# Performance work log

Measured on AMD Instinct MI355X. Metric: run time of the kernel, lower is better.

Reference implementation:

```python
import jax, jax.numpy as jnp
import numpy as np

B, N, E, M, H, OUT, F = 4, 10000, 160000, 4, 64, 64, 64


def setup_inputs() -> dict:
    key = jax.random.key(0)
    k1, k2, k3, k4, k5, k6 = jax.random.split(key, 6)
    node_fts = jax.random.normal(k1, (B, N, M, H), dtype=jnp.float32)
    hidden = jax.random.normal(k2, (B, N, M, H), dtype=jnp.float32)
    edge_fts = jax.random.normal(k3, (B, E, F), dtype=jnp.float32)
    edge_indices = jax.random.randint(k4, (B, E, 2), 0, N, dtype=jnp.int64)
    # hk.Linear params (truncated-normal-ish init approximated by scaled normal)
    W_nh = jax.random.normal(k5, (2 * H, OUT), dtype=jnp.float32) / np.sqrt(2 * H)
    b_nh = jnp.zeros((OUT,), dtype=jnp.float32)
    W_e = jax.random.normal(k6, (F, 1), dtype=jnp.float32) / np.sqrt(F)
    b_e = jnp.zeros((1,), dtype=jnp.float32)
    return {"node_fts": node_fts, "hidden": hidden, "edge_fts": edge_fts,
            "W_nh": W_nh, "b_nh": b_nh, "W_e": W_e, "b_e": b_e,
            "edge_indices": edge_indices}


def reference(node_fts, hidden, edge_fts, W_nh, b_nh, W_e, b_e, edge_indices):
    nb_nodes = node_fts.shape[1]
    src = edge_indices[..., 0]  # [B, E]
    tgt = edge_indices[..., 1]  # [B, E]
    # fuse node and hidden features, project: [B, N, M, 2H] @ [2H, OUT]
    nh = jnp.concatenate([node_fts, hidden], axis=-1)
    nh_fts = jnp.einsum('bnmc,co->bnmo', nh, W_nh) + b_nh  # [B, N, M, OUT]
    # gather per-edge source-node features along node axis
    nh_values = jnp.take_along_axis(nh_fts, src[:, :, None, None], axis=1)  # [B, E, M, OUT]
    # scalar gate per edge
    edge_coeff = jnp.einsum('bef,fo->beo', edge_fts, W_e) + b_e  # [B, E, 1]
    filtered = edge_coeff[..., None] * nh_values  # [B, E, M, OUT]
    # scatter-sum messages to target nodes, per batch element
    seg = jax.vmap(lambda d, s: jax.ops.segment_sum(d, s, num_segments=nb_nodes))
    updated_bits = seg(filtered, tgt)  # [B, N, M, OUT]
    return updated_bits
```

## Files before the change

kernel.cpp:

```cpp
#include <hip/hip_runtime.h>

#define Bc 4
#define Nc 10000
#define Ec 160000
#define NSEG (Bc * Nc)
#define NEDGE (Bc * Ec)
#define CAP 64
#define PROJ_BLOCKS 1250
#define GATE_BLOCKS 1250

typedef __attribute__((ext_vector_type(8))) short bf16x8;
typedef __attribute__((ext_vector_type(4))) float f32x4;

__device__ __forceinline__ unsigned short f2bf(float f) {
    union { float f; unsigned u; } x; x.f = f;
    return (unsigned short)((x.u + 0x7FFFu + ((x.u >> 16) & 1u)) >> 16);
}
__device__ __forceinline__ float bfhi(unsigned u) {
    union { unsigned u; float f; } x; x.u = u & 0xFFFF0000u; return x.f;
}
__device__ __forceinline__ float bflo(unsigned u) {
    union { unsigned u; float f; } x; x.u = u << 16; return x.f;
}

__device__ __forceinline__ float reduce16(float* p, int lane) {
#pragma unroll
    for (int off = 1, n = 8; off < 16; off <<= 1, n >>= 1) {
        const bool hi2 = (lane & off) != 0;
#pragma unroll
        for (int i = 0; i < 8; ++i)
            if (i < n) {
                const float keep = hi2 ? p[2 * i + 1] : p[2 * i];
                const float send = hi2 ? p[2 * i] : p[2 * i + 1];
                p[i] = keep + __shfl_xor(send, off, 64);
            }
    }
    return p[0];
}

__global__ __launch_bounds__(256) void proj_gate_kernel(
    const float* __restrict__ node, const float* __restrict__ hid,
    const float* __restrict__ Wnh, const float* __restrict__ bnh,
    unsigned short* __restrict__ nhf,
    const float* __restrict__ efts, const int* __restrict__ eidx,
    const float* __restrict__ We, const float* __restrict__ be,
    int2* __restrict__ epair, int slot_stride, int* __restrict__ cnt)
{
    __shared__ __align__(16) unsigned short wlds[8192];
    const int t = threadIdx.x;
    const int lane = t & 63;

    if (blockIdx.x < PROJ_BLOCKS) {
#pragma unroll
        for (int i = 0; i < 4; ++i) {
            const int f    = t + 256 * i;
            const int kt   = f >> 8;
            const int ct   = (f >> 6) & 3;
            const int l    = f & 63;
            const int quad = l >> 4, m = l & 15;
            const int col  = 16 * ct + m;
            const int krow = quad * 8 + 32 * kt;
            bf16x8 fr;
#pragma unroll
            for (int j = 0; j < 8; ++j)
                fr[j] = (short)f2bf(Wnh[(size_t)(krow + j) * 64 + col]);
            *(bf16x8*)(wlds + (size_t)f * 8) = fr;
        }
        __syncthreads();

        const int wv   = (int)(blockIdx.x * 4 + (t >> 6));
        const int m    = lane & 15;
        const int quad = lane >> 4;

        float bias[4];
#pragma unroll
        for (int ct = 0; ct < 4; ++ct) bias[ct] = bnh[m + 16 * ct];

        float4 lo[2][4], hi[2][4];
#pragma unroll
        for (int half = 0; half < 2; ++half) {
            const int arow = (wv * 2 + half) * 16 + m;
#pragma unroll
            for (int kt = 0; kt < 4; ++kt) {
                const int kbase = quad * 8 + 32 * kt;
                const float* pp = (kbase < 64)
                    ? (node + (size_t)arow * 64 + kbase)
                    : (hid  + (size_t)arow * 64 + (kbase - 64));
                lo[half][kt] = *(const float4*)pp;
                hi[half][kt] = *(const float4*)(pp + 4);
            }
        }

#pragma unroll
        for (int half = 0; half < 2; ++half) {
            f32x4 acc[4];
#pragma unroll
            for (int ct = 0; ct < 4; ++ct) acc[ct] = (f32x4){0.f, 0.f, 0.f, 0.f};
#pragma unroll
            for (int kt = 0; kt < 4; ++kt) {
                bf16x8 a;
                a[0] = (short)f2bf(lo[half][kt].x); a[1] = (short)f2bf(lo[half][kt].y);
                a[2] = (short)f2bf(lo[half][kt].z); a[3] = (short)f2bf(lo[half][kt].w);
                a[4] = (short)f2bf(hi[half][kt].x); a[5] = (short)f2bf(hi[half][kt].y);
                a[6] = (short)f2bf(hi[half][kt].z); a[7] = (short)f2bf(hi[half][kt].w);
#pragma unroll
                for (int ct = 0; ct < 4; ++ct) {
                    const bf16x8 bf = *(const bf16x8*)(wlds + (size_t)((kt * 4 + ct) * 64 + lane) * 8);
                    acc[ct] = __builtin_amdgcn_mfma_f32_16x16x32_bf16(a, bf, acc[ct], 0, 0, 0);
                }
            }
            const int r0 = (wv * 2 + half) * 16 + quad * 4;
#pragma unroll
            for (int ct = 0; ct < 4; ++ct) {
                const int col = m + 16 * ct;
#pragma unroll
                for (int reg = 0; reg < 4; ++reg)
                    nhf[(size_t)(r0 + reg) * 64 + col] = f2bf(acc[ct][reg] + bias[ct]);
            }
        }
    } else {
        const int w  = (int)((blockIdx.x - PROJ_BLOCKS) * 4 + (t >> 6));
        const int e0 = w * 128;
        const int b  = e0 / Ec;
        const int cb = b * Nc;
        const float4 w4 = *(const float4*)(We + (size_t)(lane & 15) * 4);
        const float be0 = be[0];
        const int perm = 4 * (lane & 15) + (lane >> 4);

        const int2 st0 = *(const int2*)(eidx + (size_t)(e0 + perm) * 2);
        const int2 st1 = *(const int2*)(eidx + (size_t)(e0 + 64 + perm) * 2);
        const int seg0 = cb + st0.y;
        const int seg1 = cb + st1.y;
        const int slot0 = atomicAdd(&cnt[seg0], 1);
        const int slot1 = atomicAdd(&cnt[seg1], 1);

        float4 v[16];
        const float* base0 = efts + (size_t)e0 * 64;
#pragma unroll
        for (int j = 0; j < 16; ++j)
            v[j] = *(const float4*)(base0 + (size_t)j * 256 + lane * 4);
        float p[16];
#pragma unroll
        for (int j = 0; j < 16; ++j)
            p[j] = v[j].x * w4.x + v[j].y * w4.y + v[j].z * w4.z + v[j].w * w4.w;

        const float* base1 = efts + (size_t)(e0 + 64) * 64;
#pragma unroll
        for (int j = 0; j < 16; ++j)
            v[j] = *(const float4*)(base1 + (size_t)j * 256 + lane * 4);

        {
            const float cval = reduce16(p, lane) + be0;
            if (slot0 < CAP)
                epair[(size_t)seg0 * slot_stride + slot0] = make_int2(st0.x, __float_as_int(cval));
        }

#pragma unroll
        for (int j = 0; j < 16; ++j)
            p[j] = v[j].x * w4.x + v[j].y * w4.y + v[j].z * w4.z + v[j].w * w4.w;

        {
            const float cval = reduce16(p, lane) + be0;
            if (slot1 < CAP)
                epair[(size_t)seg1 * slot_stride + slot1] = make_int2(st1.x, __float_as_int(cval));
        }
    }
}

__global__ __launch_bounds__(256) void gather_kernel(
    const int* __restrict__ cnt, const int2* epair, int slot_stride,
    const unsigned* __restrict__ nhf, float* out)
{
    const int lane = threadIdx.x & 63;
    int seg = (int)((blockIdx.x * blockDim.x + threadIdx.x) >> 6);
    if (seg >= NSEG) return;
    seg = __builtin_amdgcn_readfirstlane(seg);
    const int b = seg / Nc;
    const int deg = cnt[seg];
    const int end = deg < CAP ? deg : CAP;
    const int2* bp = epair + (size_t)seg * slot_stride;
    const unsigned* base = nhf + (size_t)b * Nc * 128 + lane * 2;
    const int2 my = bp[lane];

    f32x4 acc[4];
#pragma unroll
    for (int j = 0; j < 4; ++j) acc[j] = (f32x4){0.f, 0.f, 0.f, 0.f};

    int i = 0;
    for (; i + 8 <= end; i += 8) {
        int sx[8]; float cc[8]; uint2 r[8];
#pragma unroll
        for (int j = 0; j < 8; ++j) {
            sx[j] = __shfl(my.x, i + j, 64);
            cc[j] = __int_as_float(__shfl(my.y, i + j, 64));
        }
#pragma unroll
        for (int j = 0; j < 8; ++j) r[j] = *(const uint2*)(base + (size_t)sx[j] * 128);
#pragma unroll
        for (int j = 0; j < 8; ++j) {
            acc[j & 3][0] += cc[j] * bflo(r[j].x);
            acc[j & 3][1] += cc[j] * bfhi(r[j].x);
            acc[j & 3][2] += cc[j] * bflo(r[j].y);
            acc[j & 3][3] += cc[j] * bfhi(r[j].y);
        }
    }
    if (i + 4 <= end) {
        int sx[4]; float cc[4]; uint2 r[4];
#pragma unroll
        for (int j = 0; j < 4; ++j) {
            sx[j] = __shfl(my.x, i + j, 64);
            cc[j] = __int_as_float(__shfl(my.y, i + j, 64));
        }
#pragma unroll
        for (int j = 0; j < 4; ++j) r[j] = *(const uint2*)(base + (size_t)sx[j] * 128);
#pragma unroll
        for (int j = 0; j < 4; ++j) {
            acc[j][0] += cc[j] * bflo(r[j].x);
            acc[j][1] += cc[j] * bfhi(r[j].x);
            acc[j][2] += cc[j] * bflo(r[j].y);
            acc[j][3] += cc[j] * bfhi(r[j].y);
        }
        i += 4;
    }
    for (; i < end; ++i) {
        const int sx = __shfl(my.x, i, 64);
        const float cc = __int_as_float(__shfl(my.y, i, 64));
        const uint2 r = *(const uint2*)(base + (size_t)sx * 128);
        acc[0][0] += cc * bflo(r.x);
        acc[0][1] += cc * bfhi(r.x);
        acc[0][2] += cc * bflo(r.y);
        acc[0][3] += cc * bfhi(r.y);
    }
    float4 o;
    o.x = (acc[0][0] + acc[1][0]) + (acc[2][0] + acc[3][0]);
    o.y = (acc[0][1] + acc[1][1]) + (acc[2][1] + acc[3][1]);
    o.z = (acc[0][2] + acc[1][2]) + (acc[2][2] + acc[3][2]);
    o.w = (acc[0][3] + acc[1][3]) + (acc[2][3] + acc[3][3]);
    *(float4*)(out + (size_t)seg * 256 + lane * 4) = o;
}

__global__ __launch_bounds__(256) void edge_atomic_kernel(
    const float* __restrict__ efts, const int* __restrict__ eidx,
    const float* __restrict__ We, const float* __restrict__ be,
    const unsigned* __restrict__ nhf, float* __restrict__ out)
{
    const int lane = threadIdx.x & 63;
    const int eg   = (int)((blockIdx.x * blockDim.x + threadIdx.x) >> 6);
    if (eg >= NEDGE) return;
    const int b = eg / Ec;
    float c = efts[(size_t)eg * 64 + lane] * We[lane];
#pragma unroll
    for (int off = 32; off > 0; off >>= 1) c += __shfl_xor(c, off, 64);
    c += be[0];
    const int src = eidx[(size_t)eg * 2 + 0];
    const int tgt = eidx[(size_t)eg * 2 + 1];
    const uint2 r = *(const uint2*)(nhf + ((size_t)(b * Nc + src)) * 128 + lane * 2);
    float* op = out + ((size_t)(b * Nc + tgt)) * 256 + lane * 4;
    atomicAdd(op + 0, c * bflo(r.x));
    atomicAdd(op + 1, c * bfhi(r.x));
    atomicAdd(op + 2, c * bflo(r.y));
    atomicAdd(op + 3, c * bfhi(r.y));
}

extern "C" void kernel_launch(void* const* d_in, const int* in_sizes, int n_in,
                              void* d_out, int out_size, void* d_ws, size_t ws_size,
                              hipStream_t stream) {
    const float* node = (const float*)d_in[0];
    const float* hid  = (const float*)d_in[1];
    const float* efts = (const float*)d_in[2];
    const float* Wnh  = (const float*)d_in[3];
    const float* bnh  = (const float*)d_in[4];
    const float* We   = (const float*)d_in[5];
    const float* be   = (const float*)d_in[6];
    const int*   eidx = (const int*)d_in[7];
    float* out = (float*)d_out;

    unsigned* ws = (unsigned*)d_ws;
    unsigned short* nhf16 = (unsigned short*)ws;
    int* cnt = (int*)(ws + 5120000);
    const size_t ws_compact = (size_t)10280000 * 4;
    const size_t ws_minimal = (size_t)5160000 * 4;

    if (ws_size >= ws_minimal) {
        int2* epair;
        int stride;
        if (ws_size >= ws_compact) { epair = (int2*)(ws + 5160000); stride = 64; }
        else                       { epair = (int2*)d_out;          stride = 128; }
        hipMemsetAsync(cnt, 0, (size_t)NSEG * sizeof(int), stream);
        proj_gate_kernel<<<PROJ_BLOCKS + GATE_BLOCKS, 256, 0, stream>>>(
            node, hid, Wnh, bnh, nhf16, efts, eidx, We, be, epair, stride, cnt);
        gather_kernel<<<NSEG / 4, 256, 0, stream>>>(cnt, epair, stride, (const unsigned*)ws, out);
    } else {
        proj_gate_kernel<<<PROJ_BLOCKS, 256, 0, stream>>>(
            node, hid, Wnh, bnh, nhf16, efts, eidx, We, be,
            (int2*)d_out , 128, (int*)d_out );
        hipMemsetAsync(d_out, 0, (size_t)out_size * sizeof(float), stream);
        edge_atomic_kernel<<<NEDGE / 4, 256, 0, stream>>>(efts, eidx, We, be, (const unsigned*)ws, out);
    }
}
```

Measured before the change: 348.6 us.

## Rebalance per-wave work: finer proj/gate waves, gate-first order, two segments per gather wave

The projection branch now computes one 16-row tile per wave instead of two, and the gate branch handles 64 edges per wave instead of 128. Block counts double to compensate, and gate blocks are placed before projection blocks in the grid. The gather kernel now handles two target segments per wave in sequence, halving its grid. The goal is more parallelism and earlier scheduling of the atomic-heavy gate work, but it gives up the explicit load/compute overlap of the two-batch code. The fallback path now also launches the gate blocks, which do wasted work there.

Result: no change. 352.2 us (+1.0%).

```diff
diff --git a/kernel.cpp b/kernel.cpp
--- a/kernel.cpp
+++ b/kernel.cpp
@@ -6,8 +6,8 @@
 #define NSEG (Bc * Nc)
 #define NEDGE (Bc * Ec)
 #define CAP 64
-#define PROJ_BLOCKS 1250
-#define GATE_BLOCKS 1250
+#define GATE_BLOCKS 2500
+#define PROJ_BLOCKS 2500
 
 typedef __attribute__((ext_vector_type(8))) short bf16x8;
 typedef __attribute__((ext_vector_type(4))) float f32x4;
@@ -50,7 +50,7 @@
     const int t = threadIdx.x;
     const int lane = t & 63;
 
-    if (blockIdx.x < PROJ_BLOCKS) {
+    if (blockIdx.x >= GATE_BLOCKS) {
 #pragma unroll
         for (int i = 0; i < 4; ++i) {
             const int f    = t + 256 * i;
@@ -68,7 +68,7 @@
         }
         __syncthreads();
 
-        const int wv   = (int)(blockIdx.x * 4 + (t >> 6));
+        const int tile = (int)((blockIdx.x - GATE_BLOCKS) * 4 + (t >> 6));
         const int m    = lane & 15;
         const int quad = lane >> 4;
 
@@ -76,94 +76,60 @@
 #pragma unroll
         for (int ct = 0; ct < 4; ++ct) bias[ct] = bnh[m + 16 * ct];
 
-        float4 lo[2][4], hi[2][4];
-#pragma unroll
-        for (int half = 0; half < 2; ++half) {
-            const int arow = (wv * 2 + half) * 16 + m;
-#pragma unroll
-            for (int kt = 0; kt < 4; ++kt) {
-                const int kbase = quad * 8 + 32 * kt;
-                const float* pp = (kbase < 64)
-                    ? (node + (size_t)arow * 64 + kbase)
-                    : (hid  + (size_t)arow * 64 + (kbase - 64));
-                lo[half][kt] = *(const float4*)pp;
-                hi[half][kt] = *(const float4*)(pp + 4);
-            }
-        }
-
-#pragma unroll
-        for (int half = 0; half < 2; ++half) {
-            f32x4 acc[4];
-#pragma unroll
-            for (int ct = 0; ct < 4; ++ct) acc[ct] = (f32x4){0.f, 0.f, 0.f, 0.f};
-#pragma unroll
-            for (int kt = 0; kt < 4; ++kt) {
-                bf16x8 a;
-                a[0] = (short)f2bf(lo[half][kt].x); a[1] = (short)f2bf(lo[half][kt].y);
-                a[2] = (short)f2bf(lo[half][kt].z); a[3] = (short)f2bf(lo[half][kt].w);
-                a[4] = (short)f2bf(hi[half][kt].x); a[5] = (short)f2bf(hi[half][kt].y);
-                a[6] = (short)f2bf(hi[half][kt].z); a[7] = (short)f2bf(hi[half][kt].w);
-#pragma unroll
-                for (int ct = 0; ct < 4; ++ct) {
-                    const bf16x8 bf = *(const bf16x8*)(wlds + (size_t)((kt * 4 + ct) * 64 + lane) * 8);
-                    acc[ct] = __builtin_amdgcn_mfma_f32_16x16x32_bf16(a, bf, acc[ct], 0, 0, 0);
-                }
-            }
-            const int r0 = (wv * 2 + half) * 16 + quad * 4;
+        const int arow = tile * 16 + m;
+        f32x4 acc[4];
+#pragma unroll
+        for (int ct = 0; ct < 4; ++ct) acc[ct] = (f32x4){0.f, 0.f, 0.f, 0.f};
+
+#pragma unroll
+        for (int kt = 0; kt < 4; ++kt) {
+            const int kbase = quad * 8 + 32 * kt;
+            const float* pp = (kbase < 64)
+                ? (node + (size_t)arow * 64 + kbase)
+                : (hid  + (size_t)arow * 64 + (kbase - 64));
+            const float4 lo = *(const float4*)pp;
+            const float4 hi = *(const float4*)(pp + 4);
+            bf16x8 a;
+            a[0] = (short)f2bf(lo.x); a[1] = (short)f2bf(lo.y);
+            a[2] = (short)f2bf(lo.z); a[3] = (short)f2bf(lo.w);
+            a[4] = (short)f2bf(hi.x); a[5] = (short)f2bf(hi.y);
+            a[6] = (short)f2bf(hi.z); a[7] = (short)f2bf(hi.w);
 #pragma unroll
             for (int ct = 0; ct < 4; ++ct) {
-                const int col = m + 16 * ct;
-#pragma unroll
-                for (int reg = 0; reg < 4; ++reg)
-                    nhf[(size_t)(r0 + reg) * 64 + col] = f2bf(acc[ct][reg] + bias[ct]);
-            }
+                const bf16x8 bf = *(const bf16x8*)(wlds + (size_t)((kt * 4 + ct) * 64 + lane) * 8);
+                acc[ct] = __builtin_amdgcn_mfma_f32_16x16x32_bf16(a, bf, acc[ct], 0, 0, 0);
+            }
+        }
+
+        const int r0 = tile * 16 + quad * 4;
+#pragma unroll
+        for (int ct = 0; ct < 4; ++ct) {
+            const int col = m + 16 * ct;
+#pragma unroll
+            for (int reg = 0; reg < 4; ++reg)
+                nhf[(size_t)(r0 + reg) * 64 + col] = f2bf(acc[ct][reg] + bias[ct]);
         }
     } else {
-        const int w  = (int)((blockIdx.x - PROJ_BLOCKS) * 4 + (t >> 6));
-        const int e0 = w * 128;
+        const int w  = (int)(blockIdx.x * 4 + (t >> 6));
+        const int e0 = w * 64;
         const int b  = e0 / Ec;
-        const int cb = b * Nc;
+        const int perm = 4 * (lane & 15) + (lane >> 4);
+
+        const int2 st = *(const int2*)(eidx + (size_t)(e0 + perm) * 2);
+        const int seg  = b * Nc + st.y;
+        const int slot = atomicAdd(&cnt[seg], 1);
+
         const float4 w4 = *(const float4*)(We + (size_t)(lane & 15) * 4);
-        const float be0 = be[0];
-        const int perm = 4 * (lane & 15) + (lane >> 4);
-
-        const int2 st0 = *(const int2*)(eidx + (size_t)(e0 + perm) * 2);
-        const int2 st1 = *(const int2*)(eidx + (size_t)(e0 + 64 + perm) * 2);
-        const int seg0 = cb + st0.y;
-        const int seg1 = cb + st1.y;
-        const int slot0 = atomicAdd(&cnt[seg0], 1);
-        const int slot1 = atomicAdd(&cnt[seg1], 1);
-
-        float4 v[16];
-        const float* base0 = efts + (size_t)e0 * 64;
-#pragma unroll
-        for (int j = 0; j < 16; ++j)
-            v[j] = *(const float4*)(base0 + (size_t)j * 256 + lane * 4);
+        const float* base = efts + (size_t)e0 * 64;
         float p[16];
 #pragma unroll
-        for (int j = 0; j < 16; ++j)
-            p[j] = v[j].x * w4.x + v[j].y * w4.y + v[j].z * w4.z + v[j].w * w4.w;
-
-        const float* base1 = efts + (size_t)(e0 + 64) * 64;
-#pragma unroll
-        for (int j = 0; j < 16; ++j)
-            v[j] = *(const float4*)(base1 + (size_t)j * 256 + lane * 4);
-
-        {
-            const float cval = reduce16(p, lane) + be0;
-            if (slot0 < CAP)
-                epair[(size_t)seg0 * slot_stride + slot0] = make_int2(st0.x, __float_as_int(cval));
-        }
-
-#pragma unroll
-        for (int j = 0; j < 16; ++j)
-            p[j] = v[j].x * w4.x + v[j].y * w4.y + v[j].z * w4.z + v[j].w * w4.w;
-
-        {
-            const float cval = reduce16(p, lane) + be0;
-            if (slot1 < CAP)
-                epair[(size_t)seg1 * slot_stride + slot1] = make_int2(st1.x, __float_as_int(cval));
-        }
+        for (int j = 0; j < 16; ++j) {
+            const float4 v = *(const float4*)(base + (size_t)j * 256 + lane * 4);
+            p[j] = v.x * w4.x + v.y * w4.y + v.z * w4.z + v.w * w4.w;
+        }
+        const float cval = reduce16(p, lane) + be[0];
+        if (slot < CAP)
+            epair[(size_t)seg * slot_stride + slot] = make_int2(st.x, __float_as_int(cval));
     }
 }
 
@@ -172,71 +138,82 @@
     const unsigned* __restrict__ nhf, float* out)
 {
     const int lane = threadIdx.x & 63;
-    int seg = (int)((blockIdx.x * blockDim.x + threadIdx.x) >> 6);
-    if (seg >= NSEG) return;
-    seg = __builtin_amdgcn_readfirstlane(seg);
-    const int b = seg / Nc;
-    const int deg = cnt[seg];
-    const int end = deg < CAP ? deg : CAP;
-    const int2* bp = epair + (size_t)seg * slot_stride;
-    const unsigned* base = nhf + (size_t)b * Nc * 128 + lane * 2;
-    const int2 my = bp[lane];
-
-    f32x4 acc[4];
-#pragma unroll
-    for (int j = 0; j < 4; ++j) acc[j] = (f32x4){0.f, 0.f, 0.f, 0.f};
-
-    int i = 0;
-    for (; i + 8 <= end; i += 8) {
-        int sx[8]; float cc[8]; uint2 r[8];
-#pragma unroll
-        for (int j = 0; j < 8; ++j) {
-            sx[j] = __shfl(my.x, i + j, 64);
-            cc[j] = __int_as_float(__shfl(my.y, i + j, 64));
-        }
-#pragma unroll
-        for (int j = 0; j < 8; ++j) r[j] = *(const uint2*)(base + (size_t)sx[j] * 128);
-#pragma unroll
-        for (int j = 0; j < 8; ++j) {
-            acc[j & 3][0] += cc[j] * bflo(r[j].x);
-            acc[j & 3][1] += cc[j] * bfhi(r[j].x);
-            acc[j & 3][2] += cc[j] * bflo(r[j].y);
-            acc[j & 3][3] += cc[j] * bfhi(r[j].y);
-        }
-    }
-    if (i + 4 <= end) {
-        int sx[4]; float cc[4]; uint2 r[4];
-#pragma unroll
-        for (int j = 0; j < 4; ++j) {
-            sx[j] = __shfl(my.x, i + j, 64);
-            cc[j] = __int_as_float(__shfl(my.y, i + j, 64));
-        }
-#pragma unroll
-        for (int j = 0; j < 4; ++j) r[j] = *(const uint2*)(base + (size_t)sx[j] * 128);
-#pragma unroll
-        for (int j = 0; j < 4; ++j) {
-            acc[j][0] += cc[j] * bflo(r[j].x);
-            acc[j][1] += cc[j] * bfhi(r[j].x);
-            acc[j][2] += cc[j] * bflo(r[j].y);
-            acc[j][3] += cc[j] * bfhi(r[j].y);
-        }
-        i += 4;
-    }
-    for (; i < end; ++i) {
-        const int sx = __shfl(my.x, i, 64);
-        const float cc = __int_as_float(__shfl(my.y, i, 64));
-        const uint2 r = *(const uint2*)(base + (size_t)sx * 128);
-        acc[0][0] += cc * bflo(r.x);
-        acc[0][1] += cc * bfhi(r.x);
-        acc[0][2] += cc * bflo(r.y);
-        acc[0][3] += cc * bfhi(r.y);
-    }
-    float4 o;
-    o.x = (acc[0][0] + acc[1][0]) + (acc[2][0] + acc[3][0]);
-    o.y = (acc[0][1] + acc[1][1]) + (acc[2][1] + acc[3][1]);
-    o.z = (acc[0][2] + acc[1][2]) + (acc[2][2] + acc[3][2]);
-    o.w = (acc[0][3] + acc[1][3]) + (acc[2][3] + acc[3][3]);
-    *(float4*)(out + (size_t)seg * 256 + lane * 4) = o;
+    int pr = (int)((blockIdx.x * blockDim.x + threadIdx.x) >> 6);
+    if (pr >= NSEG / 2) return;
+    pr = __builtin_amdgcn_readfirstlane(pr);
+    const int seg0 = pr * 2, seg1 = pr * 2 + 1;
+
+    const int2* bp0 = epair + (size_t)seg0 * slot_stride;
+    const int2* bp1 = epair + (size_t)seg1 * slot_stride;
+    const int2 my0 = bp0[lane];
+    const int2 my1 = bp1[lane];
+    const int deg0 = cnt[seg0], deg1 = cnt[seg1];
+
+#pragma unroll
+    for (int s = 0; s < 2; ++s) {
+        const int seg = s ? seg1 : seg0;
+        const int deg = s ? deg1 : deg0;
+        const int2 my = s ? my1 : my0;
+        const int end = deg < CAP ? deg : CAP;
+        const int b = seg / Nc;
+        const unsigned* base = nhf + (size_t)b * Nc * 128 + lane * 2;
+
+        f32x4 acc[4];
+#pragma unroll
+        for (int j = 0; j < 4; ++j) acc[j] = (f32x4){0.f, 0.f, 0.f, 0.f};
+
+        int i = 0;
+        for (; i + 8 <= end; i += 8) {
+            int sx[8]; float cc[8]; uint2 r[8];
+#pragma unroll
+            for (int j = 0; j < 8; ++j) {
+                sx[j] = __shfl(my.x, i + j, 64);
+                cc[j] = __int_as_float(__shfl(my.y, i + j, 64));
+            }
+#pragma unroll
+            for (int j = 0; j < 8; ++j) r[j] = *(const uint2*)(base + (size_t)sx[j] * 128);
+#pragma unroll
+            for (int j = 0; j < 8; ++j) {
+                acc[j & 3][0] += cc[j] * bflo(r[j].x);
+                acc[j & 3][1] += cc[j] * bfhi(r[j].x);
+                acc[j & 3][2] += cc[j] * bflo(r[j].y);
+                acc[j & 3][3] += cc[j] * bfhi(r[j].y);
+            }
+        }
+        if (i + 4 <= end) {
+            int sx[4]; float cc[4]; uint2 r[4];
+#pragma unroll
+            for (int j = 0; j < 4; ++j) {
+                sx[j] = __shfl(my.x, i + j, 64);
+                cc[j] = __int_as_float(__shfl(my.y, i + j, 64));
+            }
+#pragma unroll
+            for (int j = 0; j < 4; ++j) r[j] = *(const uint2*)(base + (size_t)sx[j] * 128);
+#pragma unroll
+            for (int j = 0; j < 4; ++j) {
+                acc[j][0] += cc[j] * bflo(r[j].x);
+                acc[j][1] += cc[j] * bfhi(r[j].x);
+                acc[j][2] += cc[j] * bflo(r[j].y);
+                acc[j][3] += cc[j] * bfhi(r[j].y);
+            }
+            i += 4;
+        }
+        for (; i < end; ++i) {
+            const int sx = __shfl(my.x, i, 64);
+            const float cc = __int_as_float(__shfl(my.y, i, 64));
+            const uint2 r = *(const uint2*)(base + (size_t)sx * 128);
+            acc[0][0] += cc * bflo(r.x);
+            acc[0][1] += cc * bfhi(r.x);
+            acc[0][2] += cc * bflo(r.y);
+            acc[0][3] += cc * bfhi(r.y);
+        }
+        float4 o;
+        o.x = (acc[0][0] + acc[1][0]) + (acc[2][0] + acc[3][0]);
+        o.y = (acc[0][1] + acc[1][1]) + (acc[2][1] + acc[3][1]);
+        o.z = (acc[0][2] + acc[1][2]) + (acc[2][2] + acc[3][2]);
+        o.w = (acc[0][3] + acc[1][3]) + (acc[2][3] + acc[3][3]);
+        *(float4*)(out + (size_t)seg * 256 + lane * 4) = o;
+    }
 }
 
 __global__ __launch_bounds__(256) void edge_atomic_kernel(
@@ -287,11 +264,11 @@
         if (ws_size >= ws_compact) { epair = (int2*)(ws + 5160000); stride = 64; }
         else                       { epair = (int2*)d_out;          stride = 128; }
         hipMemsetAsync(cnt, 0, (size_t)NSEG * sizeof(int), stream);
-        proj_gate_kernel<<<PROJ_BLOCKS + GATE_BLOCKS, 256, 0, stream>>>(
+        proj_gate_kernel<<<GATE_BLOCKS + PROJ_BLOCKS, 256, 0, stream>>>(
             node, hid, Wnh, bnh, nhf16, efts, eidx, We, be, epair, stride, cnt);
-        gather_kernel<<<NSEG / 4, 256, 0, stream>>>(cnt, epair, stride, (const unsigned*)ws, out);
+        gather_kernel<<<NSEG / 8, 256, 0, stream>>>(cnt, epair, stride, (const unsigned*)ws, out);
     } else {
-        proj_gate_kernel<<<PROJ_BLOCKS, 256, 0, stream>>>(
+        proj_gate_kernel<<<GATE_BLOCKS + PROJ_BLOCKS, 256, 0, stream>>>(
             node, hid, Wnh, bnh, nhf16, efts, eidx, We, be,
             (int2*)d_out , 128, (int*)d_out );
         hipMemsetAsync(d_out, 0, (size_t)out_size * sizeof(float), stream);
```
